# Optimization experiments

Measured on AMD Instinct MI355X. Metric: run time of the kernel, lower is better.

## Reference

```python
import jax, jax.numpy as jnp
import numpy as np

N_NODES = 50000
N_EDGES = 800000
IN_C = 512
OUT_C = 256
DEC_D = 256
MASK_RATE = 0.5
NUM_MASK = int(N_NODES * MASK_RATE)


def _gcn_conv(h_in, W, b, src, dst, dinv, n):
    # PyG GCNConv: add self-loops, symmetric normalization D^-1/2 (A+I) D^-1/2
    h = h_in @ W                                   # [N, out]
    coef = (dinv[src] * dinv[dst])[:, None]        # [E, 1]
    agg = jax.ops.segment_sum(h[src] * coef, dst, num_segments=n)
    agg = agg + h * (dinv * dinv)[:, None]         # self-loop term
    return agg + b


def setup_inputs() -> dict:
    key = jax.random.key(0)
    ks = jax.random.split(key, 9)
    x = jax.random.normal(ks[0], (N_NODES, IN_C), dtype=jnp.float32)
    edge_index = jax.random.randint(ks[1], (2, N_EDGES), 0, N_NODES, dtype=jnp.int32)
    perm = jax.random.permutation(ks[2], N_NODES)
    mask_indices = perm[:NUM_MASK].astype(jnp.int32)
    mask_token = jax.random.normal(ks[3], (1, IN_C), dtype=jnp.float32)
    s_enc = 1.0 / np.sqrt(IN_C)
    enc_W = jax.random.uniform(ks[4], (IN_C, OUT_C), jnp.float32, -s_enc, s_enc)
    enc_b = jnp.zeros((OUT_C,), jnp.float32)
    s_dec = 1.0 / np.sqrt(OUT_C)
    dec_W = jax.random.uniform(ks[5], (OUT_C, DEC_D), jnp.float32, -s_dec, s_dec)
    dec_b = jnp.zeros((DEC_D,), jnp.float32)
    s_mlp = 1.0 / np.sqrt(DEC_D)
    mlp_W = jax.random.uniform(ks[6], (DEC_D, IN_C), jnp.float32, -s_mlp, s_mlp)
    mlp_b = jax.random.uniform(ks[7], (IN_C,), jnp.float32, -s_mlp, s_mlp)
    return {"x": x, "edge_index": edge_index, "mask_indices": mask_indices,
            "mask_token": mask_token, "enc_W": enc_W, "enc_b": enc_b,
            "dec_W": dec_W, "dec_b": dec_b, "mlp_W": mlp_W, "mlp_b": mlp_b}


def reference(x, edge_index, mask_indices, mask_token, enc_W, enc_b, dec_W, dec_b, mlp_W, mlp_b):
    src, dst = edge_index[0], edge_index[1]
    n = x.shape[0]
    # degree with self-loops (shared by both GCN layers)
    deg = jax.ops.segment_sum(jnp.ones((N_EDGES,), x.dtype), dst, num_segments=n) + 1.0
    dinv = jax.lax.rsqrt(deg)
    # mask nodes: replace masked rows with learned mask token
    x_masked = x.at[mask_indices].set(mask_token[0])
    # encoder: GCNConv(in_c -> out_c)
    z = _gcn_conv(x_masked, enc_W, enc_b, src, dst, dinv, n)
    # decoder: GCNConv(out_c -> dec_d) -> relu -> linear(dec_d -> in_c)
    h = jax.nn.relu(_gcn_conv(z, dec_W, dec_b, src, dst, dinv, n))
    x_recon = h @ mlp_W + mlp_b
    return (x_recon, x, mask_indices)
```

## Files before the change

kernel.cpp:

```cpp
#include <hip/hip_runtime.h>
#include <math.h>

#define NNODES 50000
#define NEDGES 800000
#define INC 512
#define OUTC 256
#define DECD 256
#define NMASK 25000

#define SCAN_B 1024
#define NSCAN ((NNODES + SCAN_B - 1) / SCAN_B)

typedef __attribute__((ext_vector_type(8))) short short8;
typedef __attribute__((ext_vector_type(4))) float f32x4;

__device__ __forceinline__ unsigned short f2bf(float f) {
    unsigned int u = __float_as_uint(f);
    u = (u + 0x7fff + ((u >> 16) & 1)) >> 16;
    return (unsigned short)u;
}
__device__ __forceinline__ float bf2f(unsigned short u) {
    return __uint_as_float(((unsigned int)u) << 16);
}


__global__ void count_deg_k(const int* __restrict__ dst, int* __restrict__ deg) {
    int e = blockIdx.x * blockDim.x + threadIdx.x;
    if (e < NEDGES) atomicAdd(&deg[dst[e]], 1);
}

__global__ __launch_bounds__(1024) void scan_part_k(const int* __restrict__ deg,
                                                    int* __restrict__ bsum,
                                                    float* __restrict__ dinv) {
    int i = blockIdx.x * SCAN_B + threadIdx.x;
    int v = (i < NNODES) ? deg[i] : 0;
    if (i < NNODES) dinv[i] = rsqrtf((float)v + 1.0f);
    int lane = threadIdx.x & 63, w = threadIdx.x >> 6;
    int s = v;
#pragma unroll
    for (int d = 32; d > 0; d >>= 1) s += __shfl_down(s, d, 64);
    __shared__ int ws[16];
    if (lane == 0) ws[w] = s;
    __syncthreads();
    if (threadIdx.x == 0) {
        int tot = 0;
#pragma unroll
        for (int j = 0; j < 16; ++j) tot += ws[j];
        bsum[blockIdx.x] = tot;
    }
}

__global__ __launch_bounds__(64) void scan_carry_k(const int* __restrict__ bsum,
                                                   int* __restrict__ bcarry,
                                                   int* __restrict__ offs) {
    int t = threadIdx.x;
    int v = (t < NSCAN) ? bsum[t] : 0;
    int incl = v;
#pragma unroll
    for (int d = 1; d < 64; d <<= 1) {
        int u = __shfl_up(incl, d, 64);
        if (t >= d) incl += u;
    }
    if (t < NSCAN) bcarry[t] = incl - v;
    if (t == 63) offs[NNODES] = incl;
}

__global__ __launch_bounds__(1024) void scan_fin_k(const int* __restrict__ deg,
                                                   const int* __restrict__ bcarry,
                                                   int* __restrict__ offs,
                                                   int* __restrict__ cursor) {
    int i = blockIdx.x * SCAN_B + threadIdx.x;
    int v = (i < NNODES) ? deg[i] : 0;
    int lane = threadIdx.x & 63, w = threadIdx.x >> 6;
    int incl = v;
#pragma unroll
    for (int d = 1; d < 64; d <<= 1) {
        int u = __shfl_up(incl, d, 64);
        if (lane >= d) incl += u;
    }
    __shared__ int ws[16];
    if (lane == 63) ws[w] = incl;
    __syncthreads();
    int carry = bcarry[blockIdx.x];
    for (int j = 0; j < w; ++j) carry += ws[j];
    int ex = carry + incl - v;
    if (i < NNODES) { offs[i] = ex; cursor[i] = ex; }
}

__global__ void fill_csr_k(const int* __restrict__ src, const int* __restrict__ dst,
                           const float* __restrict__ dinv, int* __restrict__ cursor,
                           int2* __restrict__ edges,
                           const int* __restrict__ midx, float* __restrict__ out_mask) {
    int e = blockIdx.x * blockDim.x + threadIdx.x;
    if (e >= NEDGES) return;
    if (e < NMASK) out_mask[e] = (float)midx[e];
    int s = src[e], d = dst[e];
    int pos = atomicAdd(&cursor[d], 1);
    edges[pos] = make_int2(s, __float_as_int(dinv[s] * dinv[d]));
}


__global__ void cvt_copy_k(const float4* __restrict__ in, float4* __restrict__ outx,
                           ushort4* __restrict__ outbf, int n4) {
    int i = blockIdx.x * blockDim.x + threadIdx.x;
    if (i >= n4) return;
    float4 v = in[i];
    outx[i] = v;
    ushort4 u;
    u.x = f2bf(v.x); u.y = f2bf(v.y); u.z = f2bf(v.z); u.w = f2bf(v.w);
    outbf[i] = u;
}

__global__ void wt3_k(const float* __restrict__ encW, const float* __restrict__ decW,
                      const float* __restrict__ mlpW,
                      unsigned short* __restrict__ encWt, unsigned short* __restrict__ decWt,
                      unsigned short* __restrict__ mlpWt) {
    int o = blockIdx.x * blockDim.x + threadIdx.x;
    if (o < 131072) {
        int n = o >> 9, k = o & 511;
        encWt[o] = f2bf(encW[(size_t)k * OUTC + n]);
    } else if (o < 131072 + 65536) {
        int o2 = o - 131072;
        int n = o2 >> 8, k = o2 & 255;
        decWt[o2] = f2bf(decW[(size_t)k * DECD + n]);
    } else if (o < 131072 + 65536 + 131072) {
        int o2 = o - 131072 - 65536;
        int n = o2 >> 8, k = o2 & 255;
        mlpWt[o2] = f2bf(mlpW[(size_t)k * INC + n]);
    }
}

__global__ __launch_bounds__(64) void token_k(const float* __restrict__ token,
                                              const float* __restrict__ W,
                                              float* __restrict__ outv) {
    int j = blockIdx.x;
    int l = threadIdx.x;
    float s = 0.f;
#pragma unroll
    for (int i = 0; i < INC / 64; ++i) {
        int k = i * 64 + l;
        s += token[k] * W[(size_t)k * OUTC + j];
    }
#pragma unroll
    for (int d = 32; d > 0; d >>= 1) s += __shfl_down(s, d, 64);
    if (l == 0) outv[j] = s;
}

__global__ __launch_bounds__(64) void maskfix_bf_k(const int* __restrict__ idx,
                                                   const float* __restrict__ tokh,
                                                   unsigned short* __restrict__ h1) {
    int r = idx[blockIdx.x];
    int t = threadIdx.x;
    float4 v = *(const float4*)(tokh + t * 4);
    ushort4 u;
    u.x = f2bf(v.x); u.y = f2bf(v.y); u.z = f2bf(v.z); u.w = f2bf(v.w);
    *(ushort4*)(h1 + (size_t)r * OUTC + t * 4) = u;
}


__global__ __launch_bounds__(256) void gemm_bf16_k(const unsigned short* __restrict__ A,
                                                   const unsigned short* __restrict__ Bt,
                                                   void* __restrict__ Cout,
                                                   int M, int K, int N,
                                                   const float* __restrict__ bias,
                                                   int out_bf16) {
    __shared__ unsigned short As[128 * 32];
    __shared__ unsigned short Bs[128 * 32];
    const int t = threadIdx.x;
    const int lane = t & 63, wv = t >> 6;
    const int bm = blockIdx.y * 128;
    const int bn = blockIdx.x * 128;
    const int wm = (wv >> 1) * 64, wn = (wv & 1) * 64;
    const int lr = lane & 15, lq = lane >> 4;

    f32x4 acc[4][4] = {};

    for (int k0 = 0; k0 < K; k0 += 32) {
        __syncthreads();
#pragma unroll
        for (int r = 0; r < 2; ++r) {
            int idx = r * 256 + wv * 64 + lane;
            int row = idx >> 2;
            int c8 = (idx & 3) * 8;
            int ga = bm + row;
            if (ga >= M) ga = M - 1;
            const unsigned short* gA = A + (size_t)ga * K + k0 + c8;
            const unsigned short* gB = Bt + (size_t)(bn + row) * K + k0 + c8;
            __builtin_amdgcn_global_load_lds(
                (const __attribute__((address_space(1))) unsigned int*)gA,
                (__attribute__((address_space(3))) unsigned int*)&As[(r * 256 + wv * 64) * 8],
                16, 0, 0);
            __builtin_amdgcn_global_load_lds(
                (const __attribute__((address_space(1))) unsigned int*)gB,
                (__attribute__((address_space(3))) unsigned int*)&Bs[(r * 256 + wv * 64) * 8],
                16, 0, 0);
        }
        __syncthreads();

        short8 av[4], bv[4];
#pragma unroll
        for (int mt = 0; mt < 4; ++mt)
            av[mt] = *(const short8*)&As[(wm + mt * 16 + lr) * 32 + lq * 8];
#pragma unroll
        for (int nt = 0; nt < 4; ++nt)
            bv[nt] = *(const short8*)&Bs[(wn + nt * 16 + lr) * 32 + lq * 8];
#pragma unroll
        for (int mt = 0; mt < 4; ++mt)
#pragma unroll
            for (int nt = 0; nt < 4; ++nt)
                acc[mt][nt] = __builtin_amdgcn_mfma_f32_16x16x32_bf16(
                    av[mt], bv[nt], acc[mt][nt], 0, 0, 0);
    }

    float* Cf = (float*)Cout;
    unsigned short* Cb = (unsigned short*)Cout;
#pragma unroll
    for (int nt = 0; nt < 4; ++nt) {
        int col = bn + wn + nt * 16 + lr;
        float bv_ = bias ? bias[col] : 0.f;
#pragma unroll
        for (int mt = 0; mt < 4; ++mt) {
            int row0 = bm + wm + mt * 16 + lq * 4;
#pragma unroll
            for (int reg = 0; reg < 4; ++reg) {
                int row = row0 + reg;
                if (row >= M) continue;
                float v = acc[mt][nt][reg] + bv_;
                if (out_bf16) Cb[(size_t)row * N + col] = f2bf(v);
                else          Cf[(size_t)row * N + col] = v;
            }
        }
    }
}


__global__ __launch_bounds__(256) void agg_bf_k(const unsigned short* __restrict__ h,
                                                unsigned short* __restrict__ out,
                                                const float* __restrict__ bias,
                                                const float* __restrict__ dinv,
                                                const int* __restrict__ offs,
                                                const int2* __restrict__ edges,
                                                int do_relu) {
    int node = blockIdx.x * 4 + (threadIdx.x >> 6);
    if (node >= NNODES) return;
    int t = threadIdx.x & 63;
    int beg = offs[node], end = offs[node + 1];
    float a0 = 0.f, a1 = 0.f, a2 = 0.f, a3 = 0.f;
    float b0 = 0.f, b1 = 0.f, b2 = 0.f, b3 = 0.f;
    int e = beg;
    for (; e + 2 <= end; e += 2) {
        int2 ev0 = edges[e];
        int2 ev1 = edges[e + 1];
        ushort4 v0 = *(const ushort4*)(h + (size_t)ev0.x * OUTC + t * 4);
        ushort4 v1 = *(const ushort4*)(h + (size_t)ev1.x * OUTC + t * 4);
        float c0 = __int_as_float(ev0.y);
        float c1 = __int_as_float(ev1.y);
        a0 += bf2f(v0.x) * c0; a1 += bf2f(v0.y) * c0;
        a2 += bf2f(v0.z) * c0; a3 += bf2f(v0.w) * c0;
        b0 += bf2f(v1.x) * c1; b1 += bf2f(v1.y) * c1;
        b2 += bf2f(v1.z) * c1; b3 += bf2f(v1.w) * c1;
    }
    if (e < end) {
        int2 ev = edges[e];
        ushort4 v = *(const ushort4*)(h + (size_t)ev.x * OUTC + t * 4);
        float c = __int_as_float(ev.y);
        a0 += bf2f(v.x) * c; a1 += bf2f(v.y) * c;
        a2 += bf2f(v.z) * c; a3 += bf2f(v.w) * c;
    }
    a0 += b0; a1 += b1; a2 += b2; a3 += b3;
    float di = dinv[node];
    float sc = di * di;
    ushort4 hv = *(const ushort4*)(h + (size_t)node * OUTC + t * 4);
    float4 bv = *(const float4*)(bias + t * 4);
    a0 += bf2f(hv.x) * sc + bv.x;
    a1 += bf2f(hv.y) * sc + bv.y;
    a2 += bf2f(hv.z) * sc + bv.z;
    a3 += bf2f(hv.w) * sc + bv.w;
    if (do_relu) {
        a0 = fmaxf(a0, 0.f); a1 = fmaxf(a1, 0.f);
        a2 = fmaxf(a2, 0.f); a3 = fmaxf(a3, 0.f);
    }
    ushort4 u;
    u.x = f2bf(a0); u.y = f2bf(a1); u.z = f2bf(a2); u.w = f2bf(a3);
    *(ushort4*)(out + (size_t)node * OUTC + t * 4) = u;
}


extern "C" void kernel_launch(void* const* d_in, const int* in_sizes, int n_in,
                              void* d_out, int out_size, void* d_ws, size_t ws_size,
                              hipStream_t stream) {
    const float* x    = (const float*)d_in[0];
    const int*   eidx = (const int*)d_in[1];
    const int*   midx = (const int*)d_in[2];
    const float* mtok = (const float*)d_in[3];
    const float* encW = (const float*)d_in[4];
    const float* encB = (const float*)d_in[5];
    const float* decW = (const float*)d_in[6];
    const float* decB = (const float*)d_in[7];
    const float* mlpW = (const float*)d_in[8];
    const float* mlpB = (const float*)d_in[9];
    const int* srcs = eidx;
    const int* dsts = eidx + NEDGES;

    char* ws = (char*)d_ws;
    unsigned short* x_bf  = (unsigned short*)(ws + 0);
    unsigned short* hA_bf = (unsigned short*)(ws + 51200000);
    unsigned short* hB_bf = (unsigned short*)(ws + 76800000);
    int*   deg    = (int*)  (ws + 102400000);
    float* dinv   = (float*)(ws + 102600000);
    int*   offs   = (int*)  (ws + 102800000);
    int*   cursor = (int*)  (ws + 103000064);
    int2*  edges  = (int2*) (ws + 103200064);
    float* tokh   = (float*)(ws + 109600064);
    unsigned short* encWt = (unsigned short*)(ws + 109601088);
    unsigned short* decWt = (unsigned short*)(ws + 109863232);
    unsigned short* mlpWt = (unsigned short*)(ws + 109994304);
    int*   bsum   = (int*)  (ws + 110256448);
    int*   bcarry = (int*)  (ws + 110256704);

    float* out_recon = (float*)d_out;
    float* out_x     = out_recon + (size_t)NNODES * INC;
    float* out_mask  = out_x + (size_t)NNODES * INC;

    hipMemsetAsync(deg, 0, NNODES * sizeof(int), stream);
    count_deg_k<<<(NEDGES + 255) / 256, 256, 0, stream>>>(dsts, deg);
    scan_part_k<<<NSCAN, SCAN_B, 0, stream>>>(deg, bsum, dinv);
    scan_carry_k<<<1, 64, 0, stream>>>(bsum, bcarry, offs);
    scan_fin_k<<<NSCAN, SCAN_B, 0, stream>>>(deg, bcarry, offs, cursor);
    fill_csr_k<<<(NEDGES + 255) / 256, 256, 0, stream>>>(srcs, dsts, dinv, cursor, edges,
                                                         midx, out_mask);

    token_k<<<256, 64, 0, stream>>>(mtok, encW, tokh);

    cvt_copy_k<<<(NNODES * INC / 4 + 255) / 256, 256, 0, stream>>>(
        (const float4*)x, (float4*)out_x, (ushort4*)x_bf, NNODES * INC / 4);
    wt3_k<<<(131072 + 65536 + 131072 + 255) / 256, 256, 0, stream>>>(
        encW, decW, mlpW, encWt, decWt, mlpWt);

    gemm_bf16_k<<<dim3(OUTC / 128, (NNODES + 127) / 128), 256, 0, stream>>>(
        x_bf, encWt, hA_bf, NNODES, INC, OUTC, nullptr, 1);
    maskfix_bf_k<<<NMASK, 64, 0, stream>>>(midx, tokh, hA_bf);

    agg_bf_k<<<(NNODES + 3) / 4, 256, 0, stream>>>(hA_bf, hB_bf, encB, dinv, offs, edges, 0);

    gemm_bf16_k<<<dim3(DECD / 128, (NNODES + 127) / 128), 256, 0, stream>>>(
        hB_bf, decWt, hA_bf, NNODES, OUTC, DECD, nullptr, 1);

    agg_bf_k<<<(NNODES + 3) / 4, 256, 0, stream>>>(hA_bf, hB_bf, decB, dinv, offs, edges, 1);

    gemm_bf16_k<<<dim3(INC / 128, (NNODES + 127) / 128), 256, 0, stream>>>(
        hB_bf, mlpWt, out_recon, NNODES, DECD, INC, mlpB, 0);
}
```

Before: 673.0 us.

## Merge prep kernels, fold mask-token fix into GEMM epilogue, widen aggregation loads

Degree counting, mask-index output, a new mask bitmap, the weight transpose/convert and the token projection now run as one launch. The separate maskfix kernel is gone: the first GEMM's epilogue checks the bitmap and writes the projected token for masked rows. The aggregation kernel now has each half-wave gather a different edge with 16-byte loads and combines the halves with a cross-lane shuffle. This cuts launch count and the extra scattered write pass, at the cost of a bitmap read per row in the GEMM epilogue and idle half-waves at the final store.

```diff
diff --git a/kernel.cpp b/kernel.cpp
--- a/kernel.cpp
+++ b/kernel.cpp
@@ -23,11 +23,59 @@
     return __uint_as_float(((unsigned int)u) << 16);
 }
 
-
-__global__ void count_deg_k(const int* __restrict__ dst, int* __restrict__ deg) {
-    int e = blockIdx.x * blockDim.x + threadIdx.x;
-    if (e < NEDGES) atomicAdd(&deg[dst[e]], 1);
-}
+__global__ __launch_bounds__(256) void prep_k(const int* __restrict__ dst, int* __restrict__ deg,
+                                              const int* __restrict__ midx,
+                                              float* __restrict__ out_mask,
+                                              unsigned* __restrict__ maskbits,
+                                              const float* __restrict__ encW,
+                                              const float* __restrict__ decW,
+                                              const float* __restrict__ mlpW,
+                                              unsigned short* __restrict__ encWt,
+                                              unsigned short* __restrict__ decWt,
+                                              unsigned short* __restrict__ mlpWt,
+                                              const float* __restrict__ token,
+                                              float* __restrict__ tokh) {
+    int b = blockIdx.x, tid = threadIdx.x;
+    if (b < 3125) {
+        int e = b * 256 + tid;
+        atomicAdd(&deg[dst[e]], 1);
+    } else if (b < 3223) {
+        int i = (b - 3125) * 256 + tid;
+        if (i < NMASK) {
+            int r = midx[i];
+            out_mask[i] = (float)r;
+            atomicOr(&maskbits[r >> 5], 1u << (r & 31));
+        }
+    } else if (b < 4503) {
+        int o = (b - 3223) * 256 + tid;
+        if (o < 131072) {
+            int n = o >> 9, k = o & 511;
+            encWt[o] = f2bf(encW[(size_t)k * OUTC + n]);
+        } else if (o < 196608) {
+            int o2 = o - 131072;
+            int n = o2 >> 8, k = o2 & 255;
+            decWt[o2] = f2bf(decW[(size_t)k * DECD + n]);
+        } else {
+            int o2 = o - 196608;
+            int n = o2 >> 8, k = o2 & 255;
+            mlpWt[o2] = f2bf(mlpW[(size_t)k * INC + n]);
+        }
+    } else {
+        int b2 = b - 4503;
+        int j = b2 * 4 + (tid >> 6);
+        int l = tid & 63;
+        float s = 0.f;
+#pragma unroll
+        for (int i = 0; i < INC / 64; ++i) {
+            int k = i * 64 + l;
+            s += token[k] * encW[(size_t)k * OUTC + j];
+        }
+#pragma unroll
+        for (int d = 32; d > 0; d >>= 1) s += __shfl_down(s, d, 64);
+        if (l == 0) tokh[j] = s;
+    }
+}
+
 
 __global__ __launch_bounds__(1024) void scan_part_k(const int* __restrict__ deg,
                                                     int* __restrict__ bsum,
@@ -89,16 +137,13 @@
 
 __global__ void fill_csr_k(const int* __restrict__ src, const int* __restrict__ dst,
                            const float* __restrict__ dinv, int* __restrict__ cursor,
-                           int2* __restrict__ edges,
-                           const int* __restrict__ midx, float* __restrict__ out_mask) {
+                           int2* __restrict__ edges) {
     int e = blockIdx.x * blockDim.x + threadIdx.x;
     if (e >= NEDGES) return;
-    if (e < NMASK) out_mask[e] = (float)midx[e];
     int s = src[e], d = dst[e];
     int pos = atomicAdd(&cursor[d], 1);
     edges[pos] = make_int2(s, __float_as_int(dinv[s] * dinv[d]));
 }
-
 
 __global__ void cvt_copy_k(const float4* __restrict__ in, float4* __restrict__ outx,
                            ushort4* __restrict__ outbf, int n4) {
@@ -111,59 +156,15 @@
     outbf[i] = u;
 }
 
-__global__ void wt3_k(const float* __restrict__ encW, const float* __restrict__ decW,
-                      const float* __restrict__ mlpW,
-                      unsigned short* __restrict__ encWt, unsigned short* __restrict__ decWt,
-                      unsigned short* __restrict__ mlpWt) {
-    int o = blockIdx.x * blockDim.x + threadIdx.x;
-    if (o < 131072) {
-        int n = o >> 9, k = o & 511;
-        encWt[o] = f2bf(encW[(size_t)k * OUTC + n]);
-    } else if (o < 131072 + 65536) {
-        int o2 = o - 131072;
-        int n = o2 >> 8, k = o2 & 255;
-        decWt[o2] = f2bf(decW[(size_t)k * DECD + n]);
-    } else if (o < 131072 + 65536 + 131072) {
-        int o2 = o - 131072 - 65536;
-        int n = o2 >> 8, k = o2 & 255;
-        mlpWt[o2] = f2bf(mlpW[(size_t)k * INC + n]);
-    }
-}
-
-__global__ __launch_bounds__(64) void token_k(const float* __restrict__ token,
-                                              const float* __restrict__ W,
-                                              float* __restrict__ outv) {
-    int j = blockIdx.x;
-    int l = threadIdx.x;
-    float s = 0.f;
-#pragma unroll
-    for (int i = 0; i < INC / 64; ++i) {
-        int k = i * 64 + l;
-        s += token[k] * W[(size_t)k * OUTC + j];
-    }
-#pragma unroll
-    for (int d = 32; d > 0; d >>= 1) s += __shfl_down(s, d, 64);
-    if (l == 0) outv[j] = s;
-}
-
-__global__ __launch_bounds__(64) void maskfix_bf_k(const int* __restrict__ idx,
-                                                   const float* __restrict__ tokh,
-                                                   unsigned short* __restrict__ h1) {
-    int r = idx[blockIdx.x];
-    int t = threadIdx.x;
-    float4 v = *(const float4*)(tokh + t * 4);
-    ushort4 u;
-    u.x = f2bf(v.x); u.y = f2bf(v.y); u.z = f2bf(v.z); u.w = f2bf(v.w);
-    *(ushort4*)(h1 + (size_t)r * OUTC + t * 4) = u;
-}
-
 
 __global__ __launch_bounds__(256) void gemm_bf16_k(const unsigned short* __restrict__ A,
                                                    const unsigned short* __restrict__ Bt,
                                                    void* __restrict__ Cout,
                                                    int M, int K, int N,
                                                    const float* __restrict__ bias,
-                                                   int out_bf16) {
+                                                   int out_bf16,
+                                                   const unsigned* __restrict__ maskbits,
+                                                   const float* __restrict__ tokh) {
     __shared__ unsigned short As[128 * 32];
     __shared__ unsigned short Bs[128 * 32];
     const int t = threadIdx.x;
@@ -212,12 +213,24 @@
                     av[mt], bv[nt], acc[mt][nt], 0, 0, 0);
     }
 
+    bool mrow[16];
+#pragma unroll
+    for (int mt = 0; mt < 4; ++mt)
+#pragma unroll
+        for (int reg = 0; reg < 4; ++reg) {
+            int row = bm + wm + mt * 16 + lq * 4 + reg;
+            mrow[mt * 4 + reg] = false;
+            if (maskbits && row < M)
+                mrow[mt * 4 + reg] = (maskbits[row >> 5] >> (row & 31)) & 1;
+        }
+
     float* Cf = (float*)Cout;
     unsigned short* Cb = (unsigned short*)Cout;
 #pragma unroll
     for (int nt = 0; nt < 4; ++nt) {
         int col = bn + wn + nt * 16 + lr;
         float bv_ = bias ? bias[col] : 0.f;
+        float tk = tokh ? tokh[col] : 0.f;
 #pragma unroll
         for (int mt = 0; mt < 4; ++mt) {
             int row0 = bm + wm + mt * 16 + lq * 4;
@@ -225,7 +238,7 @@
             for (int reg = 0; reg < 4; ++reg) {
                 int row = row0 + reg;
                 if (row >= M) continue;
-                float v = acc[mt][nt][reg] + bv_;
+                float v = mrow[mt * 4 + reg] ? tk : (acc[mt][nt][reg] + bv_);
                 if (out_bf16) Cb[(size_t)row * N + col] = f2bf(v);
                 else          Cf[(size_t)row * N + col] = v;
             }
@@ -244,45 +257,64 @@
     int node = blockIdx.x * 4 + (threadIdx.x >> 6);
     if (node >= NNODES) return;
     int t = threadIdx.x & 63;
+    int half = t >> 5;
+    int cb = (t & 31) * 8;
     int beg = offs[node], end = offs[node + 1];
-    float a0 = 0.f, a1 = 0.f, a2 = 0.f, a3 = 0.f;
-    float b0 = 0.f, b1 = 0.f, b2 = 0.f, b3 = 0.f;
+    float a[8] = {}, b[8] = {};
     int e = beg;
-    for (; e + 2 <= end; e += 2) {
-        int2 ev0 = edges[e];
-        int2 ev1 = edges[e + 1];
-        ushort4 v0 = *(const ushort4*)(h + (size_t)ev0.x * OUTC + t * 4);
-        ushort4 v1 = *(const ushort4*)(h + (size_t)ev1.x * OUTC + t * 4);
+    for (; e + 4 <= end; e += 4) {
+        int2 ev0 = edges[e + half];
+        int2 ev1 = edges[e + 2 + half];
+        short8 v0 = *(const short8*)(h + (size_t)ev0.x * OUTC + cb);
+        short8 v1 = *(const short8*)(h + (size_t)ev1.x * OUTC + cb);
         float c0 = __int_as_float(ev0.y);
         float c1 = __int_as_float(ev1.y);
-        a0 += bf2f(v0.x) * c0; a1 += bf2f(v0.y) * c0;
-        a2 += bf2f(v0.z) * c0; a3 += bf2f(v0.w) * c0;
-        b0 += bf2f(v1.x) * c1; b1 += bf2f(v1.y) * c1;
-        b2 += bf2f(v1.z) * c1; b3 += bf2f(v1.w) * c1;
+#pragma unroll
+        for (int j = 0; j < 8; ++j) {
+            a[j] += bf2f((unsigned short)v0[j]) * c0;
+            b[j] += bf2f((unsigned short)v1[j]) * c1;
+        }
+    }
+    if (e + 2 <= end) {
+        int2 ev = edges[e + half];
+        short8 v = *(const short8*)(h + (size_t)ev.x * OUTC + cb);
+        float c = __int_as_float(ev.y);
+#pragma unroll
+        for (int j = 0; j < 8; ++j) a[j] += bf2f((unsigned short)v[j]) * c;
+        e += 2;
     }
     if (e < end) {
         int2 ev = edges[e];
-        ushort4 v = *(const ushort4*)(h + (size_t)ev.x * OUTC + t * 4);
-        float c = __int_as_float(ev.y);
-        a0 += bf2f(v.x) * c; a1 += bf2f(v.y) * c;
-        a2 += bf2f(v.z) * c; a3 += bf2f(v.w) * c;
-    }
-    a0 += b0; a1 += b1; a2 += b2; a3 += b3;
-    float di = dinv[node];
-    float sc = di * di;
-    ushort4 hv = *(const ushort4*)(h + (size_t)node * OUTC + t * 4);
-    float4 bv = *(const float4*)(bias + t * 4);
-    a0 += bf2f(hv.x) * sc + bv.x;
-    a1 += bf2f(hv.y) * sc + bv.y;
-    a2 += bf2f(hv.z) * sc + bv.z;
-    a3 += bf2f(hv.w) * sc + bv.w;
-    if (do_relu) {
-        a0 = fmaxf(a0, 0.f); a1 = fmaxf(a1, 0.f);
-        a2 = fmaxf(a2, 0.f); a3 = fmaxf(a3, 0.f);
-    }
-    ushort4 u;
-    u.x = f2bf(a0); u.y = f2bf(a1); u.z = f2bf(a2); u.w = f2bf(a3);
-    *(ushort4*)(out + (size_t)node * OUTC + t * 4) = u;
+        short8 v = *(const short8*)(h + (size_t)ev.x * OUTC + cb);
+        float c = half ? 0.f : __int_as_float(ev.y);
+#pragma unroll
+        for (int j = 0; j < 8; ++j) a[j] += bf2f((unsigned short)v[j]) * c;
+    }
+#pragma unroll
+    for (int j = 0; j < 8; ++j) {
+        a[j] += b[j];
+        a[j] += __shfl_xor(a[j], 32, 64);
+    }
+    if (half == 0) {
+        float di = dinv[node];
+        float sc = di * di;
+        short8 hv = *(const short8*)(h + (size_t)node * OUTC + cb);
+        float4 bv0 = *(const float4*)(bias + cb);
+        float4 bv1 = *(const float4*)(bias + cb + 4);
+        float r[8];
+#pragma unroll
+        for (int j = 0; j < 8; ++j) r[j] = a[j] + bf2f((unsigned short)hv[j]) * sc;
+        r[0] += bv0.x; r[1] += bv0.y; r[2] += bv0.z; r[3] += bv0.w;
+        r[4] += bv1.x; r[5] += bv1.y; r[6] += bv1.z; r[7] += bv1.w;
+        if (do_relu) {
+#pragma unroll
+            for (int j = 0; j < 8; ++j) r[j] = fmaxf(r[j], 0.f);
+        }
+        short8 u;
+#pragma unroll
+        for (int j = 0; j < 8; ++j) u[j] = (short)f2bf(r[j]);
+        *(short8*)(out + (size_t)node * OUTC + cb) = u;
+    }
 }
 
 
@@ -306,48 +338,47 @@
     unsigned short* x_bf  = (unsigned short*)(ws + 0);
     unsigned short* hA_bf = (unsigned short*)(ws + 51200000);
     unsigned short* hB_bf = (unsigned short*)(ws + 76800000);
-    int*   deg    = (int*)  (ws + 102400000);
-    float* dinv   = (float*)(ws + 102600000);
-    int*   offs   = (int*)  (ws + 102800000);
-    int*   cursor = (int*)  (ws + 103000064);
-    int2*  edges  = (int2*) (ws + 103200064);
-    float* tokh   = (float*)(ws + 109600064);
-    unsigned short* encWt = (unsigned short*)(ws + 109601088);
-    unsigned short* decWt = (unsigned short*)(ws + 109863232);
-    unsigned short* mlpWt = (unsigned short*)(ws + 109994304);
-    int*   bsum   = (int*)  (ws + 110256448);
-    int*   bcarry = (int*)  (ws + 110256704);
+    int*      deg      = (int*)     (ws + 102400000);
+    unsigned* maskbits = (unsigned*)(ws + 102600000);
+    float*    dinv     = (float*)   (ws + 102606400);
+    int*      offs     = (int*)     (ws + 102806400);
+    int*      cursor   = (int*)     (ws + 103006464);
+    int2*     edges    = (int2*)    (ws + 103206528);
+    float*    tokh     = (float*)   (ws + 109606528);
+    unsigned short* encWt = (unsigned short*)(ws + 109607552);
+    unsigned short* decWt = (unsigned short*)(ws + 109869696);
+    unsigned short* mlpWt = (unsigned short*)(ws + 110000768);
+    int*      bsum     = (int*)     (ws + 110262912);
+    int*      bcarry   = (int*)     (ws + 110263168);
 
     float* out_recon = (float*)d_out;
     float* out_x     = out_recon + (size_t)NNODES * INC;
     float* out_mask  = out_x + (size_t)NNODES * INC;
 
-    hipMemsetAsync(deg, 0, NNODES * sizeof(int), stream);
-    count_deg_k<<<(NEDGES + 255) / 256, 256, 0, stream>>>(dsts, deg);
+    hipMemsetAsync(deg, 0, 206400, stream);
+
+    prep_k<<<4567, 256, 0, stream>>>(dsts, deg, midx, out_mask, maskbits,
+                                     encW, decW, mlpW, encWt, decWt, mlpWt,
+                                     mtok, tokh);
+
     scan_part_k<<<NSCAN, SCAN_B, 0, stream>>>(deg, bsum, dinv);
     scan_carry_k<<<1, 64, 0, stream>>>(bsum, bcarry, offs);
     scan_fin_k<<<NSCAN, SCAN_B, 0, stream>>>(deg, bcarry, offs, cursor);
-    fill_csr_k<<<(NEDGES + 255) / 256, 256, 0, stream>>>(srcs, dsts, dinv, cursor, edges,
-                                                         midx, out_mask);
-
-    token_k<<<256, 64, 0, stream>>>(mtok, encW, tokh);
+    fill_csr_k<<<(NEDGES + 255) / 256, 256, 0, stream>>>(srcs, dsts, dinv, cursor, edges);
 
     cvt_copy_k<<<(NNODES * INC / 4 + 255) / 256, 256, 0, stream>>>(
         (const float4*)x, (float4*)out_x, (ushort4*)x_bf, NNODES * INC / 4);
-    wt3_k<<<(131072 + 65536 + 131072 + 255) / 256, 256, 0, stream>>>(
-        encW, decW, mlpW, encWt, decWt, mlpWt);
 
     gemm_bf16_k<<<dim3(OUTC / 128, (NNODES + 127) / 128), 256, 0, stream>>>(
-        x_bf, encWt, hA_bf, NNODES, INC, OUTC, nullptr, 1);
-    maskfix_bf_k<<<NMASK, 64, 0, stream>>>(midx, tokh, hA_bf);
+        x_bf, encWt, hA_bf, NNODES, INC, OUTC, nullptr, 1, maskbits, tokh);
 
     agg_bf_k<<<(NNODES + 3) / 4, 256, 0, stream>>>(hA_bf, hB_bf, encB, dinv, offs, edges, 0);
 
     gemm_bf16_k<<<dim3(DECD / 128, (NNODES + 127) / 128), 256, 0, stream>>>(
-        hB_bf, decWt, hA_bf, NNODES, OUTC, DECD, nullptr, 1);
+        hB_bf, decWt, hA_bf, NNODES, OUTC, DECD, nullptr, 1, nullptr, nullptr);
 
     agg_bf_k<<<(NNODES + 3) / 4, 256, 0, stream>>>(hA_bf, hB_bf, decB, dinv, offs, edges, 1);
 
     gemm_bf16_k<<<dim3(INC / 128, (NNODES + 127) / 128), 256, 0, stream>>>(
-        hB_bf, mlpWt, out_recon, NNODES, DECD, INC, mlpB, 0);
-}
+        hB_bf, mlpWt, out_recon, NNODES, DECD, INC, mlpB, 0, nullptr, nullptr);
+}
```

After: 653.4 us. 2.9% less time.
